# Kernel tuning notes

Measured on AMD Instinct MI355X. Metric: run time of the kernel, lower is better.

The kernel has to match this reference:

```python
import jax, jax.numpy as jnp
import numpy as np

# static config (matches init_kwargs)
C, NH, WS, H, W, NQ, PS = 384, 12, 8, 56, 56, 64, 8
HD = C // NH
SCALE = HD ** -0.5
EPS = 1e-5
MLP_H = 4 * C


def _rel_pos_index():
    ch, cw = np.meshgrid(np.arange(WS), np.arange(WS), indexing='ij')
    cf = np.stack([ch.ravel(), cw.ravel()])                      # [2, WS*WS]
    rel = cf[:, :, None] - cf[:, None, :]                        # [2, N, N]
    rel = rel.transpose(1, 2, 0)
    rel[:, :, 0] += WS - 1
    rel[:, :, 1] += WS - 1
    rel[:, :, 0] *= 2 * WS - 1
    return jnp.asarray(rel.sum(-1))                              # [N, N] int

REL_IDX = _rel_pos_index()


def _ln(x, g, b):
    mu = x.mean(-1, keepdims=True)
    var = ((x - mu) ** 2).mean(-1, keepdims=True)
    return (x - mu) * jax.lax.rsqrt(var + EPS) * g + b


def setup_inputs() -> dict:
    key = jax.random.key(0)
    ks = jax.random.split(key, 24)
    B = 16
    n = lambda k, shp, s=0.02: jax.random.normal(k, shp, dtype=jnp.float32) * s
    inp = {
        'x': jax.random.normal(ks[0], (B, H * W, C), dtype=jnp.float32),
        'query_tokens': n(ks[1], (1, NQ, C)),
        'kproj_w': n(ks[2], (C, C)), 'kproj_b': jnp.zeros((C,)),
        'kbn_g': jnp.ones((C,)), 'kbn_b': jnp.zeros((C,)),
        'vproj_w': n(ks[3], (C, C)), 'vproj_b': jnp.zeros((C,)),
        'vbn_g': jnp.ones((C,)), 'vbn_b': jnp.zeros((C,)),
        'ck_w': n(ks[4], (C, C)), 'ck_b': jnp.zeros((C,)),
        'cv_w': n(ks[5], (C, C)), 'cv_b': jnp.zeros((C,)),
        'qkv_w': n(ks[6], (C, 3 * C)), 'qkv_b': jnp.zeros((3 * C,)),
        'proj_w': n(ks[7], (C, C)), 'proj_b': jnp.zeros((C,)),
        'rpb_table': n(ks[8], ((2 * WS - 1) ** 2, NH)),
        'norm1_g': jnp.ones((C,)), 'norm1_b': jnp.zeros((C,)),
        'norm2_g': jnp.ones((C,)), 'norm2_b': jnp.zeros((C,)),
        'fc1_w': n(ks[9], (C, MLP_H)), 'fc1_b': jnp.zeros((MLP_H,)),
        'fc2_w': n(ks[10], (MLP_H, C)), 'fc2_b': jnp.zeros((C,)),
    }
    return inp


def _forward(x, query_tokens, kproj_w, kproj_b, kbn_g, kbn_b, vproj_w, vproj_b,
             vbn_g, vbn_b, ck_w, ck_b, cv_w, cv_b, qkv_w, qkv_b, proj_w, proj_b,
             rpb_table, norm1_g, norm1_b, norm2_g, norm2_b, fc1_w, fc1_b, fc2_w, fc2_b):
    B, L, _ = x.shape
    shortcut = x
    xn = _ln(x, norm1_g, norm1_b)                                # [B, L, C]

    # ---- global cross attention (pooled tokens -> learnable queries) ----
    x4 = xn.reshape(B, H, W, C)
    pooled = x4.reshape(B, H // PS, PS, W // PS, PS, C).mean(axis=(2, 4))  # [B,7,7,C]
    pooled = pooled.reshape(B, (H // PS) * (W // PS), C)         # [B, 49, C]
    # conv1x1 + BatchNorm2d (eval mode, default running stats mean=0, var=1)
    bn_scale = 1.0 / jnp.sqrt(1.0 + EPS)
    key = ((pooled @ kproj_w + kproj_b) * bn_scale) * kbn_g + kbn_b
    val = ((pooled @ vproj_w + vproj_b) * bn_scale) * vbn_g + vbn_b

    q = jnp.broadcast_to(query_tokens, (B, NQ, C))
    qh = q.reshape(B, NQ, NH, HD).transpose(0, 2, 1, 3)          # [B,NH,NQ,HD]
    kh = key.reshape(B, -1, NH, HD).transpose(0, 2, 1, 3)
    vh = val.reshape(B, -1, NH, HD).transpose(0, 2, 1, 3)
    attn = jax.nn.softmax(jnp.einsum('bhqd,bhkd->bhqk', qh, kh) * SCALE, axis=-1)
    o = jnp.einsum('bhqk,bhkd->bhqd', attn, vh).transpose(0, 2, 1, 3).reshape(B, NQ, C)
    gk = (o + q) @ ck_w + ck_b                                   # [B, NQ, C]
    gv = (o + q) @ cv_w + cv_b

    # ---- windowed attention with global kv concat ----
    nW = (H // WS) * (W // WS)
    N = WS * WS
    xw = (x4.reshape(B, H // WS, WS, W // WS, WS, C)
             .transpose(0, 1, 3, 2, 4, 5)
             .reshape(B * nW, N, C))                             # [B_, N, C]
    qkv = (xw @ qkv_w + qkv_b).reshape(B * nW, N, 3, NH, HD).transpose(2, 0, 3, 1, 4)
    wq, wk, wv = qkv[0], qkv[1], qkv[2]                          # [B_, NH, N, HD]

    gkh = jnp.broadcast_to(gk.reshape(B, 1, NQ, NH, HD), (B, nW, NQ, NH, HD))
    gkh = gkh.reshape(B * nW, NQ, NH, HD).transpose(0, 2, 1, 3)  # [B_, NH, NQ, HD]
    gvh = jnp.broadcast_to(gv.reshape(B, 1, NQ, NH, HD), (B, nW, NQ, NH, HD))
    gvh = gvh.reshape(B * nW, NQ, NH, HD).transpose(0, 2, 1, 3)
    wk = jnp.concatenate([wk, gkh], axis=2)                      # [B_, NH, N+NQ, HD]
    wv = jnp.concatenate([wv, gvh], axis=2)

    logits = jnp.einsum('bhqd,bhkd->bhqk', wq * SCALE, wk)       # [B_, NH, N, N+NQ]
    rpb = rpb_table[REL_IDX.reshape(-1)].reshape(N, N, NH).transpose(2, 0, 1)  # [NH,N,N]
    logits = logits.at[:, :, :, :N].add(rpb[None])
    wattn = jax.nn.softmax(logits, axis=-1)
    ow = jnp.einsum('bhqk,bhkd->bhqd', wattn, wv).transpose(0, 2, 1, 3).reshape(B * nW, N, C)
    ow = ow @ proj_w + proj_b

    # window reverse
    xr = (ow.reshape(B, H // WS, W // WS, WS, WS, C)
             .transpose(0, 1, 3, 2, 4, 5)
             .reshape(B, H * W, C))

    x = shortcut + xr
    h = jax.nn.gelu(_ln(x, norm2_g, norm2_b) @ fc1_w + fc1_b, approximate=False)
    return x + (h @ fc2_w + fc2_b)


def reference(x, query_tokens, kproj_w, kproj_b, kbn_g, kbn_b, vproj_w, vproj_b,
              vbn_g, vbn_b, ck_w, ck_b, cv_w, cv_b, qkv_w, qkv_b, proj_w, proj_b,
              rpb_table, norm1_g, norm1_b, norm2_g, norm2_b, fc1_w, fc1_b, fc2_w, fc2_b):
    return _forward(x, query_tokens, kproj_w, kproj_b, kbn_g, kbn_b, vproj_w, vproj_b,
                    vbn_g, vbn_b, ck_w, ck_b, cv_w, cv_b, qkv_w, qkv_b, proj_w, proj_b,
                    rpb_table, norm1_g, norm1_b, norm2_g, norm2_b, fc1_w, fc1_b, fc2_w, fc2_b)
```

## Files before the change

kernel.cpp:

```cpp
#include <hip/hip_runtime.h>
#include <math.h>

typedef __attribute__((ext_vector_type(8))) __bf16 bf16x8;
typedef __attribute__((ext_vector_type(4))) float f32x4;
typedef __attribute__((ext_vector_type(8))) unsigned short u16x8;

#define DI __device__ __forceinline__

DI float b2f(unsigned short u) { return __uint_as_float(((unsigned int)u) << 16); }
DI unsigned short f2b(float f) {
    unsigned int x = __float_as_uint(f);
    x += 0x7fffu + ((x >> 16) & 1u);
    return (unsigned short)(x >> 16);
}
DI unsigned short f2b_fast(float f) {
    __bf16 h = (__bf16)f;
    return *(unsigned short*)&h;
}

DI void gl16(const unsigned short* g, unsigned short* l) {
    __builtin_amdgcn_global_load_lds(
        (const __attribute__((address_space(1))) void*)g,
        (__attribute__((address_space(3))) void*)l,
        16, 0, 0);
}

DI float gelu_f(float v) {
    float y = -1.5957691216f * v - 0.0713548163f * v * v * v;
    return v * __builtin_amdgcn_rcpf(1.f + __expf(y));
}

#define SCALE_ATT 0.17677669529663687f
#define BN_SCALE  0.9999950000374997f

__global__ __launch_bounds__(256) void cvt_all(const float* __restrict__ s0, const float* __restrict__ s1,
                                               const float* __restrict__ s2, const float* __restrict__ s3,
                                               unsigned short* __restrict__ d0, unsigned short* __restrict__ d1,
                                               unsigned short* __restrict__ d2, unsigned short* __restrict__ d3) {
    int b = blockIdx.x;
    const float* in;
    unsigned short* out;
    int Kd, Nd, i0;
    if (b < 1728)      { in = s0; out = d0; Kd = 384;  Nd = 1152; i0 = b * 256; }
    else if (b < 2304) { in = s1; out = d1; Kd = 384;  Nd = 384;  i0 = (b - 1728) * 256; }
    else if (b < 4608) { in = s2; out = d2; Kd = 384;  Nd = 1536; i0 = (b - 2304) * 256; }
    else               { in = s3; out = d3; Kd = 1536; Nd = 384;  i0 = (b - 4608) * 256; }
    int i = i0 + threadIdx.x;
    if (i < Kd * Nd) {
        int k = i / Nd, n = i % Nd;
        out[(size_t)n * Kd + k] = f2b(in[i]);
    }
}

__global__ __launch_bounds__(64) void ln_kernel(const float* __restrict__ xin,
                                                const float* __restrict__ g,
                                                const float* __restrict__ bsh,
                                                unsigned short* __restrict__ out) {
    int row = blockIdx.x;
    int t = threadIdx.x;
    size_t base = (size_t)row * 384;
    float2 v[3];
    float s = 0.f, q = 0.f;
#pragma unroll
    for (int p = 0; p < 3; ++p) {
        v[p] = *(const float2*)(xin + base + p * 128 + t * 2);
        s += v[p].x + v[p].y;
        q += v[p].x * v[p].x + v[p].y * v[p].y;
    }
#pragma unroll
    for (int off = 32; off > 0; off >>= 1) {
        s += __shfl_xor(s, off);
        q += __shfl_xor(q, off);
    }
    float mu = s * (1.f / 384.f);
    float rstd = rsqrtf(q * (1.f / 384.f) - mu * mu + 1e-5f);
#pragma unroll
    for (int p = 0; p < 3; ++p) {
        int c = p * 128 + t * 2;
        unsigned int lo16 = f2b((v[p].x - mu) * rstd * g[c] + bsh[c]);
        unsigned int hi16 = f2b((v[p].y - mu) * rstd * g[c + 1] + bsh[c + 1]);
        ((unsigned int*)(out + base + p * 128))[t] = lo16 | (hi16 << 16);
    }
}

__global__ __launch_bounds__(384) void pool_kernel(const unsigned short* __restrict__ xn,
                                                   float* __restrict__ pooled) {
    int blk = blockIdx.x;
    int b = blk / 49, pp = blk % 49;
    int ph = pp / 7, pw = pp % 7;
    int c = threadIdx.x;
    float s = 0.f;
    for (int i = 0; i < 8; ++i) {
        size_t rb = ((size_t)b * 3136 + (size_t)(ph * 8 + i) * 56 + pw * 8) * 384;
        for (int j = 0; j < 8; ++j) s += b2f(xn[rb + (size_t)j * 384 + c]);
    }
    pooled[(size_t)blk * 384 + c] = s * (1.f / 64.f);
}

__global__ __launch_bounds__(128) void kvproj_kernel(
    const float* __restrict__ pooled,
    const float* __restrict__ kw, const float* __restrict__ kb,
    const float* __restrict__ kg, const float* __restrict__ kbb,
    const float* __restrict__ vw, const float* __restrict__ vb,
    const float* __restrict__ vg, const float* __restrict__ vbb,
    float* __restrict__ keyo, float* __restrict__ valo) {
    __shared__ float row[384];
    int r = blockIdx.x;
    int t = threadIdx.x;
    for (int c = t; c < 384; c += 128) row[c] = pooled[(size_t)r * 384 + c];
    __syncthreads();
#pragma unroll
    for (int p = 0; p < 3; ++p) {
        int c = t + 128 * p;
        float aK = 0.f, aV = 0.f;
        for (int k = 0; k < 384; ++k) {
            float rv = row[k];
            aK += rv * kw[(size_t)k * 384 + c];
            aV += rv * vw[(size_t)k * 384 + c];
        }
        keyo[(size_t)r * 384 + c] = (aK + kb[c]) * BN_SCALE * kg[c] + kbb[c];
        valo[(size_t)r * 384 + c] = (aV + vb[c]) * BN_SCALE * vg[c] + vbb[c];
    }
}

__global__ __launch_bounds__(64) void rpb_expand_kernel(const float* __restrict__ rpbt,
                                                        float* __restrict__ rpb_mat) {
    int h = blockIdx.x >> 6, q = blockIdx.x & 63;
    int k = threadIdx.x;
    int i1 = q >> 3, j1 = q & 7, i2 = k >> 3, j2 = k & 7;
    rpb_mat[((size_t)h * 64 + q) * 64 + k] = rpbt[(size_t)((i1 - i2 + 7) * 15 + (j1 - j2 + 7)) * 12 + h];
}

__global__ __launch_bounds__(64) void cross_attn_kernel(const float* __restrict__ keyg,
                                                        const float* __restrict__ valg,
                                                        const float* __restrict__ qtok,
                                                        float* __restrict__ o) {
    int b = blockIdx.x / 12, h = blockIdx.x % 12;
    __shared__ float kk[49][32];
    __shared__ float vv[49][32];
    int t = threadIdx.x;
    for (int idx = t; idx < 49 * 32; idx += 64) {
        int k = idx >> 5, d = idx & 31;
        size_t gidx = ((size_t)b * 49 + k) * 384 + h * 32 + d;
        kk[k][d] = keyg[gidx];
        vv[k][d] = valg[gidx];
    }
    __syncthreads();
    float q[32];
#pragma unroll
    for (int d = 0; d < 32; ++d) q[d] = qtok[(size_t)t * 384 + h * 32 + d] * SCALE_ATT;
    float lg[49];
    float mx = -1e30f;
#pragma unroll
    for (int k = 0; k < 49; ++k) {
        float s = 0.f;
#pragma unroll
        for (int d = 0; d < 32; ++d) s += q[d] * kk[k][d];
        lg[k] = s;
        mx = fmaxf(mx, s);
    }
    float sum = 0.f;
#pragma unroll
    for (int k = 0; k < 49; ++k) { float e = expf(lg[k] - mx); lg[k] = e; sum += e; }
    float inv = 1.f / sum;
    float od[32];
#pragma unroll
    for (int d = 0; d < 32; ++d) od[d] = 0.f;
#pragma unroll
    for (int k = 0; k < 49; ++k) {
        float wgt = lg[k];
#pragma unroll
        for (int d = 0; d < 32; ++d) od[d] += wgt * vv[k][d];
    }
#pragma unroll
    for (int d = 0; d < 32; ++d) o[((size_t)b * 64 + t) * 384 + h * 32 + d] = od[d] * inv;
}

__global__ __launch_bounds__(128) void gkv_kernel(
    const float* __restrict__ o, const float* __restrict__ qtok,
    const float* __restrict__ ckw, const float* __restrict__ ckb,
    const float* __restrict__ cvw, const float* __restrict__ cvb,
    unsigned short* __restrict__ gk, unsigned short* __restrict__ gv) {
    __shared__ float row[384];
    int r = blockIdx.x;
    int n = r & 63;
    int t = threadIdx.x;
    for (int c = t; c < 384; c += 128)
        row[c] = o[(size_t)r * 384 + c] + qtok[(size_t)n * 384 + c];
    __syncthreads();
#pragma unroll
    for (int p = 0; p < 3; ++p) {
        int c = t + 128 * p;
        float aK = 0.f, aV = 0.f;
        for (int k = 0; k < 384; ++k) {
            float rv = row[k];
            aK += rv * ckw[(size_t)k * 384 + c];
            aV += rv * cvw[(size_t)k * 384 + c];
        }
        gk[(size_t)r * 384 + c] = f2b(aK + ckb[c]);
        gv[(size_t)r * 384 + c] = f2b(aV + cvb[c]);
    }
}

template <int MODE>
__global__ __launch_bounds__(256, 3) void gemm128(const unsigned short* __restrict__ A,
                                                  const unsigned short* __restrict__ BT,
                                                  const float* __restrict__ bias,
                                                  int N, int K,
                                                  void* __restrict__ outp,
                                                  const void* __restrict__ aux0) {
    __shared__ __align__(16) unsigned short As[3][128 * 32];

    int nwg = gridDim.x * gridDim.y;
    int flat = blockIdx.y * gridDim.x + blockIdx.x;
    int flat2 = (flat & 7) * (nwg >> 3) + (flat >> 3);
    int bn = flat2 % gridDim.x, bm = flat2 / gridDim.x;

    int t = threadIdx.x;
    int w = t >> 6, lane = t & 63;
    int wm = w >> 1, wn = w & 1;
    int lo = lane & 15, g = lane >> 4;

    f32x4 acc[4][4];
#pragma unroll
    for (int i = 0; i < 4; ++i)
#pragma unroll
        for (int j = 0; j < 4; ++j) acc[i][j] = f32x4{0.f, 0.f, 0.f, 0.f};

    int srow = w * 32 + (lane >> 2);
    int schunk = (((lane & 3) ^ ((srow >> 1) & 3)) << 3);
    const unsigned short* Ap0 = A + (size_t)(bm * 128 + srow) * K + schunk;
    const unsigned short* Ap1 = A + (size_t)(bm * 128 + srow + 16) * K + schunk;
    int d0 = (w * 32) * 32, d1 = (w * 32 + 16) * 32;
    int gx = ((g ^ ((lo >> 1) & 3)) << 3);

    const unsigned short* Bbase = BT + (size_t)(bn * 128 + wn * 64 + lo) * K + g * 8;
    size_t nK16 = (size_t)16 * K;
    bf16x8 Breg[3][4];

#define STAGE(buf, kb)                    \
    do {                                  \
        gl16(Ap0 + (kb), As[buf] + d0);   \
        gl16(Ap1 + (kb), As[buf] + d1);   \
    } while (0)

#define LOADB(slot, kb)                                                        \
    do {                                                                       \
        _Pragma("unroll")                                                      \
        for (int n = 0; n < 4; ++n)                                            \
            Breg[slot][n] = *(const bf16x8*)(Bbase + (size_t)n * nK16 + (kb)); \
    } while (0)

#define WAIT6() asm volatile("s_waitcnt vmcnt(6)" ::: "memory")
#define WAIT0() asm volatile("s_waitcnt vmcnt(0)" ::: "memory")

#define COMPUTE(slot)                                                                    \
    do {                                                                                 \
        bf16x8 af[4];                                                                    \
        _Pragma("unroll")                                                                \
        for (int m = 0; m < 4; ++m)                                                      \
            af[m] = *(const bf16x8*)(As[slot] + (wm * 64 + m * 16 + lo) * 32 + gx);      \
        __builtin_amdgcn_s_setprio(1);                                                   \
        _Pragma("unroll")                                                                \
        for (int m = 0; m < 4; ++m)                                                      \
            _Pragma("unroll")                                                            \
            for (int n = 0; n < 4; ++n)                                                  \
                acc[m][n] = __builtin_amdgcn_mfma_f32_16x16x32_bf16(af[m], Breg[slot][n],\
                                                                    acc[m][n], 0, 0, 0); \
        __builtin_amdgcn_s_setprio(0);                                                   \
    } while (0)

    STAGE(0, 0);
    LOADB(0, 0);
    STAGE(1, 32);
    LOADB(1, 32);

    int nt = K >> 5;
    for (int tt = 0; tt < nt; tt += 3) {
        if (tt + 1 < nt) WAIT6(); else WAIT0();
        __builtin_amdgcn_s_barrier();
        if (tt + 2 < nt) { STAGE(2, (tt + 2) * 32); LOADB(2, (tt + 2) * 32); }
        COMPUTE(0);
        if (tt + 2 < nt) WAIT6(); else WAIT0();
        __builtin_amdgcn_s_barrier();
        if (tt + 3 < nt) { STAGE(0, (tt + 3) * 32); LOADB(0, (tt + 3) * 32); }
        COMPUTE(1);
        if (tt + 3 < nt) WAIT6(); else WAIT0();
        __builtin_amdgcn_s_barrier();
        if (tt + 4 < nt) { STAGE(1, (tt + 4) * 32); LOADB(1, (tt + 4) * 32); }
        COMPUTE(2);
    }
#undef STAGE
#undef LOADB
#undef WAIT6
#undef WAIT0
#undef COMPUTE

    int r0 = bm * 128 + wm * 64 + g * 4;
    int c0 = bn * 128 + wn * 64 + lo;
    int wgc = bm * 2 + wm;
    int bC = wgc / 49, winC = wgc % 49;
    int whC = winC / 7, wwC = winC % 7;
    int lC = (whC << 3) * 56 + (wwC << 3);
    size_t rowbaseC = (size_t)bC * 3136;
#pragma unroll
    for (int m = 0; m < 4; ++m)
#pragma unroll
        for (int n = 0; n < 4; ++n)
#pragma unroll
            for (int j = 0; j < 4; ++j) {
                int r = r0 + m * 16 + j;
                int c = c0 + n * 16;
                float v = acc[m][n][j] + bias[c];
                if (MODE == 0) {
                    ((unsigned short*)outp)[(size_t)r * N + c] = f2b(v);
                } else if (MODE == 1) {
                    int nn = m * 16 + (g << 2) + j;
                    int l = lC + (nn >> 3) * 56 + (nn & 7);
                    size_t idx = (rowbaseC + l) * 384 + c;
                    ((float*)outp)[idx] = ((const float*)aux0)[idx] + v;
                } else if (MODE == 2) {
                    ((unsigned short*)outp)[(size_t)r * N + c] = f2b(gelu_f(v));
                } else {
                    float res = ((const float*)aux0)[(size_t)r * 384 + c];
                    ((float*)outp)[(size_t)r * N + c] = v + res;
                }
            }
}

__global__ __launch_bounds__(64, 2) void win_attn_mfma(const unsigned short* __restrict__ qkv,
                                                       const unsigned short* __restrict__ gkb,
                                                       const unsigned short* __restrict__ gvb,
                                                       const float* __restrict__ rpb_mat,
                                                       unsigned short* __restrict__ ow) {
    int blk = blockIdx.x;
    int wg = blk / 12, h = blk % 12;
    int b = wg / 49, win = wg % 49;
    int wh = win / 7, ww = win % 7;
    int lane = threadIdx.x;
    int lo = lane & 15, g = lane >> 4;

    __shared__ __align__(16) unsigned short VT[32 * 136];
    __shared__ __align__(16) unsigned short PL[64 * 40];

    size_t qkvbase = (size_t)b * 3136 * 1152;
    int lbase = ((wh << 3)) * 56 + (ww << 3);

    {
        int n = lane;
        int l = lbase + (n >> 3) * 56 + (n & 7);
        const unsigned short* vp = qkv + qkvbase + (size_t)l * 1152 + 768 + h * 32;
        u16x8 v0 = *(const u16x8*)(vp);
        u16x8 v1 = *(const u16x8*)(vp + 8);
        u16x8 v2 = *(const u16x8*)(vp + 16);
        u16x8 v3 = *(const u16x8*)(vp + 24);
#pragma unroll
        for (int j = 0; j < 8; ++j) {
            VT[(0 + j) * 136 + n]  = v0[j];
            VT[(8 + j) * 136 + n]  = v1[j];
            VT[(16 + j) * 136 + n] = v2[j];
            VT[(24 + j) * 136 + n] = v3[j];
        }
        const unsigned short* gp = gvb + ((size_t)b * 64 + n) * 384 + h * 32;
        v0 = *(const u16x8*)(gp);
        v1 = *(const u16x8*)(gp + 8);
        v2 = *(const u16x8*)(gp + 16);
        v3 = *(const u16x8*)(gp + 24);
#pragma unroll
        for (int j = 0; j < 8; ++j) {
            VT[(0 + j) * 136 + 64 + n]  = v0[j];
            VT[(8 + j) * 136 + 64 + n]  = v1[j];
            VT[(16 + j) * 136 + 64 + n] = v2[j];
            VT[(24 + j) * 136 + 64 + n] = v3[j];
        }
    }

    bf16x8 qf[4];
#pragma unroll
    for (int qt = 0; qt < 4; ++qt) {
        int n = qt * 16 + lo;
        int l = lbase + (n >> 3) * 56 + (n & 7);
        qf[qt] = *(const bf16x8*)(qkv + qkvbase + (size_t)l * 1152 + h * 32 + g * 8);
    }

    f32x4 S[4][8];
#pragma unroll
    for (int qt = 0; qt < 4; ++qt)
#pragma unroll
        for (int t = 0; t < 8; ++t) S[qt][t] = f32x4{0.f, 0.f, 0.f, 0.f};

#pragma unroll
    for (int t = 0; t < 8; ++t) {
        bf16x8 kf;
        if (t < 4) {
            int key = t * 16 + lo;
            int l = lbase + (key >> 3) * 56 + (key & 7);
            kf = *(const bf16x8*)(qkv + qkvbase + (size_t)l * 1152 + 384 + h * 32 + g * 8);
        } else {
            int gkey = (t - 4) * 16 + lo;
            kf = *(const bf16x8*)(gkb + ((size_t)b * 64 + gkey) * 384 + h * 32 + g * 8);
        }
#pragma unroll
        for (int qt = 0; qt < 4; ++qt)
            S[qt][t] = __builtin_amdgcn_mfma_f32_16x16x32_bf16(qf[qt], kf, S[qt][t], 0, 0, 0);
    }

    const float* rb_h = rpb_mat + (size_t)h * 4096;
    float mx[4][4];
#pragma unroll
    for (int qt = 0; qt < 4; ++qt)
#pragma unroll
        for (int j = 0; j < 4; ++j) mx[qt][j] = -1e30f;

#pragma unroll
    for (int qt = 0; qt < 4; ++qt) {
#pragma unroll
        for (int t = 0; t < 8; ++t) {
#pragma unroll
            for (int j = 0; j < 4; ++j) {
                float v = S[qt][t][j] * SCALE_ATT;
                if (t < 4) v += rb_h[(qt * 16 + g * 4 + j) * 64 + t * 16 + lo];
                S[qt][t][j] = v;
                mx[qt][j] = fmaxf(mx[qt][j], v);
            }
        }
    }
#pragma unroll
    for (int qt = 0; qt < 4; ++qt)
#pragma unroll
        for (int j = 0; j < 4; ++j) {
#pragma unroll
            for (int m = 1; m <= 8; m <<= 1)
                mx[qt][j] = fmaxf(mx[qt][j], __shfl_xor(mx[qt][j], m));
        }

    float sm[4][4];
#pragma unroll
    for (int qt = 0; qt < 4; ++qt)
#pragma unroll
        for (int j = 0; j < 4; ++j) sm[qt][j] = 0.f;
#pragma unroll
    for (int qt = 0; qt < 4; ++qt)
#pragma unroll
        for (int t = 0; t < 8; ++t)
#pragma unroll
            for (int j = 0; j < 4; ++j) {
                float p = __expf(S[qt][t][j] - mx[qt][j]);
                S[qt][t][j] = p;
                sm[qt][j] += p;
            }
#pragma unroll
    for (int qt = 0; qt < 4; ++qt)
#pragma unroll
        for (int j = 0; j < 4; ++j) {
#pragma unroll
            for (int m = 1; m <= 8; m <<= 1)
                sm[qt][j] += __shfl_xor(sm[qt][j], m);
        }
    float inv[4][4];
#pragma unroll
    for (int qt = 0; qt < 4; ++qt)
#pragma unroll
        for (int j = 0; j < 4; ++j) inv[qt][j] = 1.f / sm[qt][j];

    f32x4 O[4][2];
#pragma unroll
    for (int qt = 0; qt < 4; ++qt)
#pragma unroll
        for (int dt = 0; dt < 2; ++dt) O[qt][dt] = f32x4{0.f, 0.f, 0.f, 0.f};

#pragma unroll
    for (int c = 0; c < 4; ++c) {
        __syncthreads();
#pragma unroll
        for (int qt = 0; qt < 4; ++qt) {
            int qb = qt * 16 + g * 4;
#pragma unroll
            for (int half = 0; half < 2; ++half) {
                int t = 2 * c + half;
#pragma unroll
                for (int j = 0; j < 4; ++j)
                    PL[(qb + j) * 40 + half * 16 + lo] = f2b_fast(S[qt][t][j]);
            }
        }
        __syncthreads();
#pragma unroll
        for (int qt = 0; qt < 4; ++qt) {
            bf16x8 pa = *(const bf16x8*)(PL + (qt * 16 + lo) * 40 + g * 8);
#pragma unroll
            for (int dt = 0; dt < 2; ++dt) {
                bf16x8 vb = *(const bf16x8*)(VT + (dt * 16 + lo) * 136 + c * 32 + g * 8);
                O[qt][dt] = __builtin_amdgcn_mfma_f32_16x16x32_bf16(pa, vb, O[qt][dt], 0, 0, 0);
            }
        }
    }

#pragma unroll
    for (int qt = 0; qt < 4; ++qt)
#pragma unroll
        for (int dt = 0; dt < 2; ++dt)
#pragma unroll
            for (int j = 0; j < 4; ++j) {
                int q = qt * 16 + g * 4 + j;
                int d = dt * 16 + lo;
                ow[((size_t)wg * 64 + q) * 384 + h * 32 + d] = f2b_fast(O[qt][dt][j] * inv[qt][j]);
            }
}

static const size_t OFF_XN   = 0;
static const size_t OFF_QKV  = 38535168;
static const size_t OFF_OW   = 154140672;
static const size_t OFF_X2   = 192675840;
static const size_t OFF_PL   = 269746176;
static const size_t OFF_KEY  = 270950400;
static const size_t OFF_VAL  = 272154624;
static const size_t OFF_O    = 273358848;
static const size_t OFF_GK   = 274931712;
static const size_t OFF_GV   = 276504576;
static const size_t OFF_QKVW = 278077440;
static const size_t OFF_PRJW = 278962176;
static const size_t OFF_FC1W = 279257088;
static const size_t OFF_FC2W = 280436736;

extern "C" void kernel_launch(void* const* d_in, const int* in_sizes, int n_in,
                              void* d_out, int out_size, void* d_ws, size_t ws_size,
                              hipStream_t stream) {
    const float* x      = (const float*)d_in[0];
    const float* qtok   = (const float*)d_in[1];
    const float* kprojw = (const float*)d_in[2];
    const float* kprojb = (const float*)d_in[3];
    const float* kbng   = (const float*)d_in[4];
    const float* kbnb   = (const float*)d_in[5];
    const float* vprojw = (const float*)d_in[6];
    const float* vprojb = (const float*)d_in[7];
    const float* vbng   = (const float*)d_in[8];
    const float* vbnb   = (const float*)d_in[9];
    const float* ckw    = (const float*)d_in[10];
    const float* ckb    = (const float*)d_in[11];
    const float* cvw    = (const float*)d_in[12];
    const float* cvb    = (const float*)d_in[13];
    const float* qkvw   = (const float*)d_in[14];
    const float* qkvb   = (const float*)d_in[15];
    const float* projw  = (const float*)d_in[16];
    const float* projb  = (const float*)d_in[17];
    const float* rpbt   = (const float*)d_in[18];
    const float* n1g    = (const float*)d_in[19];
    const float* n1b    = (const float*)d_in[20];
    const float* n2g    = (const float*)d_in[21];
    const float* n2b    = (const float*)d_in[22];
    const float* fc1w   = (const float*)d_in[23];
    const float* fc1b   = (const float*)d_in[24];
    const float* fc2w   = (const float*)d_in[25];
    const float* fc2b   = (const float*)d_in[26];

    char* wsb = (char*)d_ws;
    unsigned short* xn     = (unsigned short*)(wsb + OFF_XN);
    unsigned short* qkvbf  = (unsigned short*)(wsb + OFF_QKV);
    unsigned short* owbf   = (unsigned short*)(wsb + OFF_OW);
    float* x2      = (float*)(wsb + OFF_X2);
    float* pooled  = (float*)(wsb + OFF_PL);
    float* rpb_mat = (float*)(wsb + OFF_PL);
    float* keyg    = (float*)(wsb + OFF_KEY);
    float* valg    = (float*)(wsb + OFF_VAL);
    float* obuf    = (float*)(wsb + OFF_O);
    unsigned short* gkb = (unsigned short*)(wsb + OFF_GK);
    unsigned short* gvb = (unsigned short*)(wsb + OFF_GV);
    unsigned short* qkvw_t = (unsigned short*)(wsb + OFF_QKVW);
    unsigned short* prjw_t = (unsigned short*)(wsb + OFF_PRJW);
    unsigned short* fc1w_t = (unsigned short*)(wsb + OFF_FC1W);
    unsigned short* fc2w_t = (unsigned short*)(wsb + OFF_FC2W);
    unsigned short* ln2out = (unsigned short*)(wsb + OFF_XN);
    unsigned short* hbuf   = (unsigned short*)(wsb + OFF_QKV);

    cvt_all<<<6912, 256, 0, stream>>>(qkvw, projw, fc1w, fc2w, qkvw_t, prjw_t, fc1w_t, fc2w_t);
    ln_kernel<<<50176, 64, 0, stream>>>(x, n1g, n1b, xn);
    pool_kernel<<<784, 384, 0, stream>>>(xn, pooled);
    kvproj_kernel<<<784, 128, 0, stream>>>(pooled, kprojw, kprojb, kbng, kbnb,
                                           vprojw, vprojb, vbng, vbnb, keyg, valg);
    rpb_expand_kernel<<<768, 64, 0, stream>>>(rpbt, rpb_mat);
    cross_attn_kernel<<<192, 64, 0, stream>>>(keyg, valg, qtok, obuf);
    gkv_kernel<<<1024, 128, 0, stream>>>(obuf, qtok, ckw, ckb, cvw, cvb, gkb, gvb);
    gemm128<0><<<dim3(9, 392), 256, 0, stream>>>(xn, qkvw_t, qkvb, 1152, 384, qkvbf, nullptr);
    win_attn_mfma<<<9408, 64, 0, stream>>>(qkvbf, gkb, gvb, rpb_mat, owbf);
    gemm128<1><<<dim3(3, 392), 256, 0, stream>>>(owbf, prjw_t, projb, 384, 384, x2, x);
    ln_kernel<<<50176, 64, 0, stream>>>(x2, n2g, n2b, ln2out);
    gemm128<2><<<dim3(12, 392), 256, 0, stream>>>(ln2out, fc1w_t, fc1b, 1536, 384, hbuf, nullptr);
    gemm128<3><<<dim3(3, 392), 256, 0, stream>>>(hbuf, fc2w_t, fc2b, 384, 1536, (float*)d_out, x2);
}
```

Before: 812.1 us.

## Stage B tiles through LDS with a four-deep async pipeline in gemm128

The B operand is now staged into shared memory with async global-to-LDS loads, using the same swizzled layout as A. It no longer goes straight into per-wave registers. This removes duplicate global reads of B across the wm waves and frees the registers that held B. The pipeline grows from three to four stages, with vmcnt waits adjusted to the four loads each stage now issues. In exchange, shared memory per block doubles and the occupancy hint drops from 3 to 2 blocks, which may cut latency hiding.

After: 754.2 us. -7.1%, faster.

```diff
diff --git a/kernel.cpp b/kernel.cpp
--- a/kernel.cpp
+++ b/kernel.cpp
@@ -203,13 +203,14 @@
 }
 
 template <int MODE>
-__global__ __launch_bounds__(256, 3) void gemm128(const unsigned short* __restrict__ A,
+__global__ __launch_bounds__(256, 2) void gemm128(const unsigned short* __restrict__ A,
                                                   const unsigned short* __restrict__ BT,
                                                   const float* __restrict__ bias,
                                                   int N, int K,
                                                   void* __restrict__ outp,
                                                   const void* __restrict__ aux0) {
-    __shared__ __align__(16) unsigned short As[3][128 * 32];
+    __shared__ __align__(16) unsigned short As[4][128 * 32];
+    __shared__ __align__(16) unsigned short Bs[4][128 * 32];
 
     int nwg = gridDim.x * gridDim.y;
     int flat = blockIdx.y * gridDim.x + blockIdx.x;
@@ -231,69 +232,77 @@
     int schunk = (((lane & 3) ^ ((srow >> 1) & 3)) << 3);
     const unsigned short* Ap0 = A + (size_t)(bm * 128 + srow) * K + schunk;
     const unsigned short* Ap1 = A + (size_t)(bm * 128 + srow + 16) * K + schunk;
+    const unsigned short* Bp0 = BT + (size_t)(bn * 128 + srow) * K + schunk;
+    const unsigned short* Bp1 = BT + (size_t)(bn * 128 + srow + 16) * K + schunk;
     int d0 = (w * 32) * 32, d1 = (w * 32 + 16) * 32;
+
     int gx = ((g ^ ((lo >> 1) & 3)) << 3);
-
-    const unsigned short* Bbase = BT + (size_t)(bn * 128 + wn * 64 + lo) * K + g * 8;
-    size_t nK16 = (size_t)16 * K;
-    bf16x8 Breg[3][4];
 
 #define STAGE(buf, kb)                    \
     do {                                  \
         gl16(Ap0 + (kb), As[buf] + d0);   \
         gl16(Ap1 + (kb), As[buf] + d1);   \
+        gl16(Bp0 + (kb), Bs[buf] + d0);   \
+        gl16(Bp1 + (kb), Bs[buf] + d1);   \
     } while (0)
 
-#define LOADB(slot, kb)                                                        \
-    do {                                                                       \
-        _Pragma("unroll")                                                      \
-        for (int n = 0; n < 4; ++n)                                            \
-            Breg[slot][n] = *(const bf16x8*)(Bbase + (size_t)n * nK16 + (kb)); \
+#define WAIT8() asm volatile("s_waitcnt vmcnt(8)" ::: "memory")
+#define WAIT4() asm volatile("s_waitcnt vmcnt(4)" ::: "memory")
+#define WAIT0() asm volatile("s_waitcnt vmcnt(0)" ::: "memory")
+#define WAITK(k)                             \
+    do {                                     \
+        if ((k) + 2 < nt) WAIT8();           \
+        else if ((k) + 1 < nt) WAIT4();      \
+        else WAIT0();                        \
     } while (0)
 
-#define WAIT6() asm volatile("s_waitcnt vmcnt(6)" ::: "memory")
-#define WAIT0() asm volatile("s_waitcnt vmcnt(0)" ::: "memory")
-
-#define COMPUTE(slot)                                                                    \
+#define COMPUTE(buf)                                                                     \
     do {                                                                                 \
-        bf16x8 af[4];                                                                    \
+        bf16x8 af[4], bfv[4];                                                            \
         _Pragma("unroll")                                                                \
         for (int m = 0; m < 4; ++m)                                                      \
-            af[m] = *(const bf16x8*)(As[slot] + (wm * 64 + m * 16 + lo) * 32 + gx);      \
+            af[m] = *(const bf16x8*)(As[buf] + (wm * 64 + m * 16 + lo) * 32 + gx);       \
+        _Pragma("unroll")                                                                \
+        for (int n = 0; n < 4; ++n)                                                      \
+            bfv[n] = *(const bf16x8*)(Bs[buf] + (wn * 64 + n * 16 + lo) * 32 + gx);      \
         __builtin_amdgcn_s_setprio(1);                                                   \
         _Pragma("unroll")                                                                \
         for (int m = 0; m < 4; ++m)                                                      \
             _Pragma("unroll")                                                            \
             for (int n = 0; n < 4; ++n)                                                  \
-                acc[m][n] = __builtin_amdgcn_mfma_f32_16x16x32_bf16(af[m], Breg[slot][n],\
+                acc[m][n] = __builtin_amdgcn_mfma_f32_16x16x32_bf16(af[m], bfv[n],       \
                                                                     acc[m][n], 0, 0, 0); \
         __builtin_amdgcn_s_setprio(0);                                                   \
     } while (0)
 
     STAGE(0, 0);
-    LOADB(0, 0);
     STAGE(1, 32);
-    LOADB(1, 32);
+    STAGE(2, 64);
 
     int nt = K >> 5;
-    for (int tt = 0; tt < nt; tt += 3) {
-        if (tt + 1 < nt) WAIT6(); else WAIT0();
+    for (int tt = 0; tt < nt; tt += 4) {
+        WAITK(tt);
         __builtin_amdgcn_s_barrier();
-        if (tt + 2 < nt) { STAGE(2, (tt + 2) * 32); LOADB(2, (tt + 2) * 32); }
+        if (tt + 3 < nt) STAGE(3, (tt + 3) * 32);
         COMPUTE(0);
-        if (tt + 2 < nt) WAIT6(); else WAIT0();
+        WAITK(tt + 1);
         __builtin_amdgcn_s_barrier();
-        if (tt + 3 < nt) { STAGE(0, (tt + 3) * 32); LOADB(0, (tt + 3) * 32); }
+        if (tt + 4 < nt) STAGE(0, (tt + 4) * 32);
         COMPUTE(1);
-        if (tt + 3 < nt) WAIT6(); else WAIT0();
+        WAITK(tt + 2);
         __builtin_amdgcn_s_barrier();
-        if (tt + 4 < nt) { STAGE(1, (tt + 4) * 32); LOADB(1, (tt + 4) * 32); }
+        if (tt + 5 < nt) STAGE(1, (tt + 5) * 32);
         COMPUTE(2);
+        WAITK(tt + 3);
+        __builtin_amdgcn_s_barrier();
+        if (tt + 6 < nt) STAGE(2, (tt + 6) * 32);
+        COMPUTE(3);
     }
 #undef STAGE
-#undef LOADB
-#undef WAIT6
+#undef WAIT8
+#undef WAIT4
 #undef WAIT0
+#undef WAITK
 #undef COMPUTE
 
     int r0 = bm * 128 + wm * 64 + g * 4;
```
